# Kernel tuning notes

Hardware: AMD Instinct MI355X
Metric: run time of the kernel (lower is better)

The kernel has to match this reference:

```python
import jax, jax.numpy as jnp
import numpy as np

SEQ, BATCH, IN_DIM, HID, OUT = 512, 256, 300, 256, 2


def setup_inputs() -> dict:
    key = jax.random.key(0)
    ks = jax.random.split(key, 7)
    s_ih = 1.0 / np.sqrt(HID)
    return {
        "x": jax.random.normal(ks[0], (SEQ, BATCH, IN_DIM), jnp.float32),
        "W_ih": jax.random.uniform(ks[1], (HID, IN_DIM), jnp.float32, -s_ih, s_ih),
        "W_hh": jax.random.uniform(ks[2], (HID, HID), jnp.float32, -s_ih, s_ih),
        "b_ih": jax.random.uniform(ks[3], (HID,), jnp.float32, -s_ih, s_ih),
        "b_hh": jax.random.uniform(ks[4], (HID,), jnp.float32, -s_ih, s_ih),
        "W_fc": jax.random.uniform(ks[5], (OUT, HID), jnp.float32, -s_ih, s_ih),
        "b_fc": jax.random.uniform(ks[6], (OUT,), jnp.float32, -s_ih, s_ih),
    }


def reference(x, W_ih, W_hh, b_ih, b_hh, W_fc, b_fc):
    # Precompute input projection for all timesteps at once: [T, B, H]
    xp = jnp.einsum('tbi,hi->tbh', x, W_ih) + b_ih + b_hh

    def step(h, xt):
        h_new = jnp.tanh(xt + h @ W_hh.T)
        return h_new, None

    h0 = jnp.zeros((x.shape[1], W_hh.shape[0]), x.dtype)
    hT, _ = jax.lax.scan(step, h0, xp)  # hT: [B, H]
    # Dropout(0.3) is identity in eval mode.
    logits = hT @ W_fc.T + b_fc  # [B, 2]
    return jax.nn.log_softmax(logits, axis=-1)
```

## Files before the change

kernel.cpp:

```cpp
#include <hip/hip_runtime.h>
#include <hip/hip_bf16.h>
#include <cstdint>
#include <cstddef>

#define SEQ 512
#define BATCH 256
#define IN_DIM 300
#define HID 256

typedef __attribute__((ext_vector_type(8))) short bf16x8;
typedef __attribute__((ext_vector_type(4))) float f32x4;

__device__ __forceinline__ unsigned short f2bf(float f) {
  union { float f; unsigned int u; } v; v.f = f;
  unsigned int u = v.u;
  return (unsigned short)((u + 0x7fffu + ((u >> 16) & 1u)) >> 16);
}
__device__ __forceinline__ unsigned short f2bf_fast(float f) {
  union { float f; unsigned int u; } v; v.f = f;
  return (unsigned short)((v.u + 0x8000u) >> 16);
}
__device__ __forceinline__ float bitsf(unsigned int u) {
  union { unsigned int u; float f; } v; v.u = u; return v.f;
}
__device__ __forceinline__ unsigned int cvtpk(float lo, float hi) {
  union { __hip_bfloat162 h; unsigned int u; } c;
  c.h = __float22bfloat162_rn(make_float2(lo, hi));
  return c.u;
}
__device__ __forceinline__ bf16x8 cvt8(float a0,float a1,float a2,float a3,
                                       float a4,float a5,float a6,float a7) {
  union { __hip_bfloat162 h2[4]; bf16x8 v; } c;
  c.h2[0] = __float22bfloat162_rn(make_float2(a0, a1));
  c.h2[1] = __float22bfloat162_rn(make_float2(a2, a3));
  c.h2[2] = __float22bfloat162_rn(make_float2(a4, a5));
  c.h2[3] = __float22bfloat162_rn(make_float2(a6, a7));
  return c.v;
}
__device__ __forceinline__ void barrier_lgkm() {
  asm volatile("s_waitcnt lgkmcnt(0)" ::: "memory");
  __builtin_amdgcn_s_barrier();
  asm volatile("" ::: "memory");
}

__global__ __launch_bounds__(256) void conv_wih(const float* __restrict__ w,
                                                unsigned short* __restrict__ w_bf) {
  int idx = blockIdx.x * 256 + threadIdx.x;
  int j    = idx & 7;
  int l15  = (idx >> 3) & 15;
  int quad = (idx >> 7) & 3;
  int t    = idx >> 9;
  int n16  = t / 10;
  int kc   = t - n16 * 10;
  int n = n16 * 16 + l15;
  int k = kc * 32 + quad * 8 + j;
  float v = (k < IN_DIM) ? w[n * IN_DIM + k] : 0.f;
  w_bf[idx] = f2bf(v);
}

__device__ __forceinline__ void win_gemm(const unsigned int* __restrict__ a_lds,
    unsigned int* __restrict__ xpbuf, const bf16x8 wfi[2][10],
    float kb0, float kb1, int wave, int l15, int quad)
{
  f32x4 acc[2][2];
  #pragma unroll
  for (int mt = 0; mt < 2; ++mt) {
    acc[mt][0] = (f32x4){0.f,0.f,0.f,0.f};
    acc[mt][1] = (f32x4){0.f,0.f,0.f,0.f};
  }
  #pragma unroll
  for (int kc = 0; kc < 10; ++kc) {
    bf16x8 afr0 = *(const bf16x8*)&a_lds[(     l15) * 164 + kc*16 + quad*4];
    bf16x8 afr1 = *(const bf16x8*)&a_lds[(16 + l15) * 164 + kc*16 + quad*4];
    acc[0][0] = __builtin_amdgcn_mfma_f32_16x16x32_bf16(afr0, wfi[0][kc], acc[0][0], 0, 0, 0);
    acc[0][1] = __builtin_amdgcn_mfma_f32_16x16x32_bf16(afr0, wfi[1][kc], acc[0][1], 0, 0, 0);
    acc[1][0] = __builtin_amdgcn_mfma_f32_16x16x32_bf16(afr1, wfi[0][kc], acc[1][0], 0, 0, 0);
    acc[1][1] = __builtin_amdgcn_mfma_f32_16x16x32_bf16(afr1, wfi[1][kc], acc[1][1], 0, 0, 0);
  }
  #pragma unroll
  for (int nt = 0; nt < 2; ++nt) {
    const float kb = nt ? kb1 : kb0;
    const int tid_s = wave*64 + nt*16 + l15;
    #pragma unroll
    for (int mt = 0; mt < 2; ++mt) {
      const int idx = (mt*4 + quad) * 512 + tid_s;
      float y0 = fmaf(2.0f, acc[mt][nt][0], kb);
      float y1 = fmaf(2.0f, acc[mt][nt][1], kb);
      float y2 = fmaf(2.0f, acc[mt][nt][2], kb);
      float y3 = fmaf(2.0f, acc[mt][nt][3], kb);
      xpbuf[idx]      = cvtpk(y0, y1);
      xpbuf[idx + 32] = cvtpk(y2, y3);
    }
  }
}

__device__ __forceinline__ void win_stage(unsigned int* __restrict__ a_lds,
    const float4* __restrict__ xr, const int* __restrict__ sidx, int tid)
{
  #pragma unroll
  for (int i = 0; i < 5; ++i)
    if (i < 4 || tid < 352) {
      uint2 pk2;
      pk2.x = cvtpk(xr[i].x, xr[i].y);
      pk2.y = cvtpk(xr[i].z, xr[i].w);
      *(uint2*)&a_lds[sidx[i]] = pk2;
    }
}

__global__ __launch_bounds__(512, 2) void rnn_all(const float* __restrict__ x,
    const unsigned short* __restrict__ w_bf, const float* __restrict__ b_ih,
    const float* __restrict__ b_hh, const float* __restrict__ W_hh,
    const float* __restrict__ W_fc, const float* __restrict__ b_fc,
    float* __restrict__ out)
{
  __shared__ alignas(16) unsigned int   xpbuf[8 * 512];
  __shared__ alignas(16) unsigned int   a_lds[32 * 164];
  __shared__ alignas(16) unsigned short hbuf[2][1088];

  const int tid  = threadIdx.x;
  const int wave = tid >> 6;
  const int lane = tid & 63;
  const int l15  = lane & 15;
  const int quad = lane >> 4;
  const int g    = blockIdx.x;
  const int c0   = wave * 32;

  bf16x8 wfh[2][8];
  #pragma unroll
  for (int nt = 0; nt < 2; ++nt) {
    const int n = c0 + nt*16 + l15;
    #pragma unroll
    for (int kc = 0; kc < 8; ++kc) {
      const float* src = W_hh + n*HID + kc*32 + quad*8;
      float4 p0 = *(const float4*)src;
      float4 p1 = *(const float4*)(src + 4);
      wfh[nt][kc] = cvt8(p0.x,p0.y,p0.z,p0.w,p1.x,p1.y,p1.z,p1.w);
    }
  }
  bf16x8 wfi[2][10];
  #pragma unroll
  for (int nt = 0; nt < 2; ++nt) {
    const unsigned short* wp =
        w_bf + ((size_t)((wave*2 + nt)*10)*4 + quad)*128 + (size_t)l15*8;
    #pragma unroll
    for (int kc = 0; kc < 10; ++kc)
      wfi[nt][kc] = *(const bf16x8*)(wp + (size_t)kc*512);
  }
  const float kb0 = 2.0f * (b_ih[c0 + l15]      + b_hh[c0 + l15]);
  const float kb1 = 2.0f * (b_ih[c0 + 16 + l15] + b_hh[c0 + 16 + l15]);

  unsigned int voff[5]; int sidx[5];
  #pragma unroll
  for (int i = 0; i < 5; ++i) {
    const int e = tid + i * 512;
    const int row = e / 75;
    const int c4  = e - row * 75;
    const int t_loc = row >> 2, b_loc = row & 3;
    voff[i] = (unsigned)(((t_loc * 256 + 4 * g + b_loc) * 300 + c4 * 4) * 4);
    sidx[i] = row * 164 + c4 * 2;
  }

  const int rb    = (quad >> 1) * 2;
  const int col_e = c0 + (quad & 1) * 16 + l15;
  const int abase = (l15 & 3) * 272 + quad * 8;

  for (int i = tid; i < 1088; i += 512) hbuf[0][i] = 0;
  if (tid < 320) a_lds[(tid / 10) * 164 + 150 + (tid % 10)] = 0;

  float4 xr[5];
  #pragma unroll
  for (int i = 0; i < 5; ++i)
    if (i < 4 || tid < 352)
      xr[i] = *(const float4*)((const char*)x + voff[i]);
  __syncthreads();
  win_stage(a_lds, xr, sidx, tid);
  barrier_lgkm();
  win_gemm(a_lds, xpbuf, wfi, kb0, kb1, wave, l15, quad);
  barrier_lgkm();

  const size_t WSTRIDE = (size_t)8 * 256 * 300 * 4;

  for (int w = 0; w < 64; ++w) {
    const char* pn = (const char*)x + (size_t)(w + 1) * WSTRIDE;
    #pragma unroll
    for (int j = 0; j < 8; ++j) {
      if (j == 0 && w < 63) {
        #pragma unroll
        for (int i = 0; i < 5; ++i)
          if (i < 4 || tid < 352)
            xr[i] = *(const float4*)(pn + voff[i]);
      }
      const int cur = j & 1;
      const unsigned int xqj = xpbuf[j * 512 + tid];
      bf16x8 afr[8];
      #pragma unroll
      for (int kc = 0; kc < 8; ++kc)
        afr[kc] = *(const bf16x8*)&hbuf[cur][abase + kc*32];
      f32x4 a0A = (f32x4){0.f,0.f,0.f,0.f}, a0B = a0A, a1A = a0A, a1B = a0A;
      #pragma unroll
      for (int kc = 0; kc < 8; kc += 2) {
        a0A = __builtin_amdgcn_mfma_f32_16x16x32_bf16(afr[kc],   wfh[0][kc],   a0A, 0, 0, 0);
        a1A = __builtin_amdgcn_mfma_f32_16x16x32_bf16(afr[kc],   wfh[1][kc],   a1A, 0, 0, 0);
        a0B = __builtin_amdgcn_mfma_f32_16x16x32_bf16(afr[kc+1], wfh[0][kc+1], a0B, 0, 0, 0);
        a1B = __builtin_amdgcn_mfma_f32_16x16x32_bf16(afr[kc+1], wfh[1][kc+1], a1B, 0, 0, 0);
      }
      if (j == 5 && w < 63)
        win_stage(a_lds, xr, sidx, tid);
      f32x4 acc0 = a0A + a0B;
      f32x4 acc1 = a1A + a1B;
      f32x4 a = (quad & 1) ? acc1 : acc0;
      float s0 = (quad >> 1) ? a[2] : a[0];
      float s1 = (quad >> 1) ? a[3] : a[1];
      float xv0 = bitsf(xqj << 16);
      float xv1 = bitsf(xqj & 0xffff0000u);
      float y0 = fmaf(2.0f, s0, xv0);
      float y1 = fmaf(2.0f, s1, xv1);
      float h0 = fmaf(-2.0f, __builtin_amdgcn_rcpf(__expf(y0) + 1.0f), 1.0f);
      float h1 = fmaf(-2.0f, __builtin_amdgcn_rcpf(__expf(y1) + 1.0f), 1.0f);
      if (w == 63 && j == 7) {
        float* fcb = (float*)xpbuf;
        fcb[ rb      * 256 + col_e] = h0;
        fcb[(rb + 1) * 256 + col_e] = h1;
      } else {
        hbuf[1 - cur][ rb      * 272 + col_e] = f2bf_fast(h0);
        hbuf[1 - cur][(rb + 1) * 272 + col_e] = f2bf_fast(h1);
      }
      barrier_lgkm();
    }
    if (w < 63) {
      win_gemm(a_lds, xpbuf, wfi, kb0, kb1, wave, l15, quad);
      barrier_lgkm();
    }
  }

  if (wave < 4) {
    const float* fcb = (const float*)xpbuf + wave * 256;
    float s0 = 0.f, s1 = 0.f;
    #pragma unroll
    for (int j0 = 0; j0 < HID; j0 += 64) {
      float h = fcb[j0 + lane];
      s0 += h * W_fc[j0 + lane];
      s1 += h * W_fc[HID + j0 + lane];
    }
    #pragma unroll
    for (int off = 32; off > 0; off >>= 1) {
      s0 += __shfl_xor(s0, off, 64);
      s1 += __shfl_xor(s1, off, 64);
    }
    if (lane == 0) {
      const int b = g * 4 + wave;
      float l0 = s0 + b_fc[0], l1 = s1 + b_fc[1];
      float m = fmaxf(l0, l1);
      float lse = m + logf(expf(l0 - m) + expf(l1 - m));
      out[b*2 + 0] = l0 - lse;
      out[b*2 + 1] = l1 - lse;
    }
  }
}

extern "C" void kernel_launch(void* const* d_in, const int* in_sizes, int n_in,
                              void* d_out, int out_size, void* d_ws, size_t ws_size,
                              hipStream_t stream) {
  const float* x    = (const float*)d_in[0];
  const float* W_ih = (const float*)d_in[1];
  const float* W_hh = (const float*)d_in[2];
  const float* b_ih = (const float*)d_in[3];
  const float* b_hh = (const float*)d_in[4];
  const float* W_fc = (const float*)d_in[5];
  const float* b_fc = (const float*)d_in[6];
  float* out = (float*)d_out;

  const size_t wb_bytes = (size_t)256 * 320 * 2;
  if (ws_size < wb_bytes) return;
  unsigned short* w_bf = (unsigned short*)d_ws;

  hipLaunchKernelGGL(conv_wih, dim3(320), dim3(256), 0, stream, W_ih, w_bf);
  hipLaunchKernelGGL(rnn_all,  dim3(64),  dim3(512), 0, stream,
                     x, w_bf, b_ih, b_hh, W_hh, W_fc, b_fc, out);
}
```

Measured before the change: 530.1 us.

## Interleave next-window input GEMM with recurrent steps using double-buffered LDS

Double-buffers the input-projection output (xpbuf, with a padded row stride) and the staged x tile (a_lds). The next window's input GEMM is split into five chunks that run between the recurrent MFMA steps, so it is no longer a serialized phase with its own barrier. The x prefetch now runs two windows ahead. This hides the GEMM latency inside the latency-bound recurrence, at the cost of more LDS and more registers (the accumulators stay live). The occupancy hint of 2 in launch_bounds is also dropped.

```diff
diff --git a/kernel.cpp b/kernel.cpp
--- a/kernel.cpp
+++ b/kernel.cpp
@@ -7,6 +7,8 @@
 #define BATCH 256
 #define IN_DIM 300
 #define HID 256
+#define XPROW 520
+#define ABUF  5248
 
 typedef __attribute__((ext_vector_type(8))) short bf16x8;
 typedef __attribute__((ext_vector_type(4))) float f32x4;
@@ -58,43 +60,42 @@
   w_bf[idx] = f2bf(v);
 }
 
-__device__ __forceinline__ void win_gemm(const unsigned int* __restrict__ a_lds,
-    unsigned int* __restrict__ xpbuf, const bf16x8 wfi[2][10],
-    float kb0, float kb1, int wave, int l15, int quad)
+__device__ __forceinline__ void gemm_chunk(const unsigned int* __restrict__ buf,
+    f32x4 (&gacc)[2][2], const bf16x8 wfi[2][10], int kc, int l15, int quad)
 {
-  f32x4 acc[2][2];
-  #pragma unroll
-  for (int mt = 0; mt < 2; ++mt) {
-    acc[mt][0] = (f32x4){0.f,0.f,0.f,0.f};
-    acc[mt][1] = (f32x4){0.f,0.f,0.f,0.f};
-  }
-  #pragma unroll
-  for (int kc = 0; kc < 10; ++kc) {
-    bf16x8 afr0 = *(const bf16x8*)&a_lds[(     l15) * 164 + kc*16 + quad*4];
-    bf16x8 afr1 = *(const bf16x8*)&a_lds[(16 + l15) * 164 + kc*16 + quad*4];
-    acc[0][0] = __builtin_amdgcn_mfma_f32_16x16x32_bf16(afr0, wfi[0][kc], acc[0][0], 0, 0, 0);
-    acc[0][1] = __builtin_amdgcn_mfma_f32_16x16x32_bf16(afr0, wfi[1][kc], acc[0][1], 0, 0, 0);
-    acc[1][0] = __builtin_amdgcn_mfma_f32_16x16x32_bf16(afr1, wfi[0][kc], acc[1][0], 0, 0, 0);
-    acc[1][1] = __builtin_amdgcn_mfma_f32_16x16x32_bf16(afr1, wfi[1][kc], acc[1][1], 0, 0, 0);
-  }
+  #pragma unroll
+  for (int k2 = 0; k2 < 2; ++k2) {
+    const int kk = kc + k2;
+    bf16x8 afr0 = *(const bf16x8*)&buf[(     l15) * 164 + kk*16 + quad*4];
+    bf16x8 afr1 = *(const bf16x8*)&buf[(16 + l15) * 164 + kk*16 + quad*4];
+    gacc[0][0] = __builtin_amdgcn_mfma_f32_16x16x32_bf16(afr0, wfi[0][kk], gacc[0][0], 0, 0, 0);
+    gacc[0][1] = __builtin_amdgcn_mfma_f32_16x16x32_bf16(afr0, wfi[1][kk], gacc[0][1], 0, 0, 0);
+    gacc[1][0] = __builtin_amdgcn_mfma_f32_16x16x32_bf16(afr1, wfi[0][kk], gacc[1][0], 0, 0, 0);
+    gacc[1][1] = __builtin_amdgcn_mfma_f32_16x16x32_bf16(afr1, wfi[1][kk], gacc[1][1], 0, 0, 0);
+  }
+}
+__device__ __forceinline__ void gemm_epi(const f32x4 (&gacc)[2][2],
+    unsigned int* __restrict__ xp_wr, float kb0, float kb1,
+    int wave, int l15, int quad)
+{
   #pragma unroll
   for (int nt = 0; nt < 2; ++nt) {
     const float kb = nt ? kb1 : kb0;
     const int tid_s = wave*64 + nt*16 + l15;
     #pragma unroll
     for (int mt = 0; mt < 2; ++mt) {
-      const int idx = (mt*4 + quad) * 512 + tid_s;
-      float y0 = fmaf(2.0f, acc[mt][nt][0], kb);
-      float y1 = fmaf(2.0f, acc[mt][nt][1], kb);
-      float y2 = fmaf(2.0f, acc[mt][nt][2], kb);
-      float y3 = fmaf(2.0f, acc[mt][nt][3], kb);
-      xpbuf[idx]      = cvtpk(y0, y1);
-      xpbuf[idx + 32] = cvtpk(y2, y3);
-    }
-  }
-}
-
-__device__ __forceinline__ void win_stage(unsigned int* __restrict__ a_lds,
+      const int idx = (mt*4 + quad) * XPROW + tid_s;
+      float y0 = fmaf(2.0f, gacc[mt][nt][0], kb);
+      float y1 = fmaf(2.0f, gacc[mt][nt][1], kb);
+      float y2 = fmaf(2.0f, gacc[mt][nt][2], kb);
+      float y3 = fmaf(2.0f, gacc[mt][nt][3], kb);
+      xp_wr[idx]      = cvtpk(y0, y1);
+      xp_wr[idx + 32] = cvtpk(y2, y3);
+    }
+  }
+}
+
+__device__ __forceinline__ void win_stage(unsigned int* __restrict__ buf,
     const float4* __restrict__ xr, const int* __restrict__ sidx, int tid)
 {
   #pragma unroll
@@ -103,18 +104,18 @@
       uint2 pk2;
       pk2.x = cvtpk(xr[i].x, xr[i].y);
       pk2.y = cvtpk(xr[i].z, xr[i].w);
-      *(uint2*)&a_lds[sidx[i]] = pk2;
-    }
-}
-
-__global__ __launch_bounds__(512, 2) void rnn_all(const float* __restrict__ x,
+      *(uint2*)&buf[sidx[i]] = pk2;
+    }
+}
+
+__global__ __launch_bounds__(512) void rnn_all(const float* __restrict__ x,
     const unsigned short* __restrict__ w_bf, const float* __restrict__ b_ih,
     const float* __restrict__ b_hh, const float* __restrict__ W_hh,
     const float* __restrict__ W_fc, const float* __restrict__ b_fc,
     float* __restrict__ out)
 {
-  __shared__ alignas(16) unsigned int   xpbuf[8 * 512];
-  __shared__ alignas(16) unsigned int   a_lds[32 * 164];
+  __shared__ alignas(16) unsigned int   xpbuf[2 * 8 * XPROW];
+  __shared__ alignas(16) unsigned int   a_lds[2 * ABUF];
   __shared__ alignas(16) unsigned short hbuf[2][1088];
 
   const int tid  = threadIdx.x;
@@ -165,7 +166,13 @@
   const int abase = (l15 & 3) * 272 + quad * 8;
 
   for (int i = tid; i < 1088; i += 512) hbuf[0][i] = 0;
-  if (tid < 320) a_lds[(tid / 10) * 164 + 150 + (tid % 10)] = 0;
+  for (int i = tid; i < 640; i += 512) {
+    const int b   = i / 320;
+    const int rem = i - b * 320;
+    a_lds[b*ABUF + (rem/10)*164 + 150 + (rem%10)] = 0;
+  }
+
+  const size_t WSTRIDE = (size_t)8 * 256 * 300 * 4;
 
   float4 xr[5];
   #pragma unroll
@@ -174,24 +181,44 @@
       xr[i] = *(const float4*)((const char*)x + voff[i]);
   __syncthreads();
   win_stage(a_lds, xr, sidx, tid);
+  #pragma unroll
+  for (int i = 0; i < 5; ++i)
+    if (i < 4 || tid < 352)
+      xr[i] = *(const float4*)((const char*)x + WSTRIDE + voff[i]);
   barrier_lgkm();
-  win_gemm(a_lds, xpbuf, wfi, kb0, kb1, wave, l15, quad);
+  {
+    f32x4 gacc[2][2];
+    gacc[0][0] = (f32x4){0.f,0.f,0.f,0.f}; gacc[0][1] = gacc[0][0];
+    gacc[1][0] = gacc[0][0];               gacc[1][1] = gacc[0][0];
+    #pragma unroll
+    for (int kc = 0; kc < 10; kc += 2)
+      gemm_chunk(a_lds, gacc, wfi, kc, l15, quad);
+    gemm_epi(gacc, xpbuf, kb0, kb1, wave, l15, quad);
+  }
+  win_stage(a_lds + ABUF, xr, sidx, tid);
   barrier_lgkm();
 
-  const size_t WSTRIDE = (size_t)8 * 256 * 300 * 4;
-
-  for (int w = 0; w < 64; ++w) {
-    const char* pn = (const char*)x + (size_t)(w + 1) * WSTRIDE;
+  f32x4 gacc[2][2];
+  for (int W = 0; W < 64; ++W) {
+    const unsigned int* xp_rd = xpbuf + (W & 1) * (8 * XPROW);
+    unsigned int*       xp_wr = xpbuf + ((W + 1) & 1) * (8 * XPROW);
+    const unsigned int* gbuf  = a_lds + ((W + 1) & 1) * ABUF;
+    unsigned int*       sbuf  = a_lds + (W & 1) * ABUF;
+    const char* pn = (const char*)x + (size_t)(W + 2) * WSTRIDE;
     #pragma unroll
     for (int j = 0; j < 8; ++j) {
-      if (j == 0 && w < 63) {
+      if (j == 0 && W < 62) {
         #pragma unroll
         for (int i = 0; i < 5; ++i)
           if (i < 4 || tid < 352)
             xr[i] = *(const float4*)(pn + voff[i]);
       }
+      if (j == 0 && W < 63) {
+        gacc[0][0] = (f32x4){0.f,0.f,0.f,0.f}; gacc[0][1] = gacc[0][0];
+        gacc[1][0] = gacc[0][0];               gacc[1][1] = gacc[0][0];
+      }
       const int cur = j & 1;
-      const unsigned int xqj = xpbuf[j * 512 + tid];
+      const unsigned int xqj = xp_rd[j * XPROW + tid];
       bf16x8 afr[8];
       #pragma unroll
       for (int kc = 0; kc < 8; ++kc)
@@ -204,8 +231,10 @@
         a0B = __builtin_amdgcn_mfma_f32_16x16x32_bf16(afr[kc+1], wfh[0][kc+1], a0B, 0, 0, 0);
         a1B = __builtin_amdgcn_mfma_f32_16x16x32_bf16(afr[kc+1], wfh[1][kc+1], a1B, 0, 0, 0);
       }
-      if (j == 5 && w < 63)
-        win_stage(a_lds, xr, sidx, tid);
+      if (j < 5 && W < 63)
+        gemm_chunk(gbuf, gacc, wfi, 2*j, l15, quad);
+      if (j == 5 && W < 62)
+        win_stage(sbuf, xr, sidx, tid);
       f32x4 acc0 = a0A + a0B;
       f32x4 acc1 = a1A + a1B;
       f32x4 a = (quad & 1) ? acc1 : acc0;
@@ -217,7 +246,9 @@
       float y1 = fmaf(2.0f, s1, xv1);
       float h0 = fmaf(-2.0f, __builtin_amdgcn_rcpf(__expf(y0) + 1.0f), 1.0f);
       float h1 = fmaf(-2.0f, __builtin_amdgcn_rcpf(__expf(y1) + 1.0f), 1.0f);
-      if (w == 63 && j == 7) {
+      if (j == 7 && W < 63)
+        gemm_epi(gacc, xp_wr, kb0, kb1, wave, l15, quad);
+      if (W == 63 && j == 7) {
         float* fcb = (float*)xpbuf;
         fcb[ rb      * 256 + col_e] = h0;
         fcb[(rb + 1) * 256 + col_e] = h1;
@@ -225,10 +256,6 @@
         hbuf[1 - cur][ rb      * 272 + col_e] = f2bf_fast(h0);
         hbuf[1 - cur][(rb + 1) * 272 + col_e] = f2bf_fast(h1);
       }
-      barrier_lgkm();
-    }
-    if (w < 63) {
-      win_gemm(a_lds, xpbuf, wfi, kb0, kb1, wave, l15, quad);
       barrier_lgkm();
     }
   }
```

New measurement: 528.3 us. About the same (-0.3%).
